# Performance work log

Measured on AMD Instinct MI355X. Metric: run time of the kernel, lower is better.

Reference implementation:

```python
import jax, jax.numpy as jnp
import numpy as np

B = 8192
FEAT = 7680
HID = 512
LOC = 4
N_SCENES = 72


def setup_inputs() -> dict:
    key = jax.random.key(0)
    ks = jax.random.split(key, 12)
    s = lambda fan_in: 1.0 / np.sqrt(fan_in)
    inp = {
        "feat": jax.random.normal(ks[0], (B, FEAT), dtype=jnp.float32),
        "scene_idx": jax.random.randint(ks[1], (B,), 0, N_SCENES, dtype=jnp.int64),
        # visual_fc1: Linear(7680 -> 512)  (torch layout: W[out, in])
        "W1": jax.random.uniform(ks[2], (HID, FEAT), jnp.float32, -s(FEAT), s(FEAT)),
        "b1": jax.random.uniform(ks[3], (HID,), jnp.float32, -s(FEAT), s(FEAT)),
        # localization_fc: Linear(512 -> 512), ReLU, Linear(512 -> 4)
        "W2": jax.random.uniform(ks[4], (HID, HID), jnp.float32, -s(HID), s(HID)),
        "b2": jax.random.uniform(ks[5], (HID,), jnp.float32, -s(HID), s(HID)),
        "W3": jax.random.uniform(ks[6], (LOC, HID), jnp.float32, -s(HID), s(HID)),
        "b3": jax.random.uniform(ks[7], (LOC,), jnp.float32, -s(HID), s(HID)),
        # per-scene 2x2 affine (with bias) and 2x2 rotation (no bias)
        "xyW": jax.random.uniform(ks[8], (N_SCENES, 2, 2), jnp.float32, -s(2), s(2)),
        "xyb": jax.random.uniform(ks[9], (N_SCENES, 2), jnp.float32, -s(2), s(2)),
        "tW": jax.random.uniform(ks[10], (N_SCENES, 2, 2), jnp.float32, -s(2), s(2)),
    }
    return inp


def reference(feat, scene_idx, W1, b1, W2, b2, W3, b3, xyW, xyb, tW):
    # visual_fc1: Flatten (already flat) -> Linear -> ReLU
    h = jax.nn.relu(feat @ W1.T + b1)                 # [B, HID]
    # localization_fc: Linear -> ReLU -> Linear
    h = jax.nn.relu(h @ W2.T + b2)                    # [B, HID]
    shared = h @ W3.T + b3                            # [B, 4]
    # per-scene routed 2x2 linears: gather weights per sample, apply, "scatter" is
    # implicit since every row gets exactly one scene's transform.
    sidx = scene_idx.astype(jnp.int32)
    Wxy = xyW[sidx]                                   # [B, 2, 2]
    bxy = xyb[sidx]                                   # [B, 2]
    Wt = tW[sidx]                                     # [B, 2, 2]
    xy = jnp.einsum("boi,bi->bo", Wxy, shared[:, :2]) + bxy
    t = jnp.einsum("boi,bi->bo", Wt, shared[:, 2:])
    return jnp.concatenate([xy, t], axis=1)           # [B, 4]
```

## Files before the change

### kernel.cpp

```cpp
#include <hip/hip_runtime.h>
#include <stdint.h>
#include <stddef.h>

#define BROWS 8192
#define FEATK 7680
#define HIDN  512

typedef __attribute__((ext_vector_type(8))) __bf16 bf16x8;
typedef __attribute__((ext_vector_type(4))) float f32x4;

__device__ __forceinline__ unsigned short f2b(float f) {
  unsigned int u = __float_as_uint(f);
  unsigned int r = (u + 0x7FFFu + ((u >> 16) & 1u)) >> 16;
  return (unsigned short)r;
}

__global__ void cvt_kernel(const float* __restrict__ src, unsigned short* __restrict__ dst, int n4) {
  int i = blockIdx.x * blockDim.x + threadIdx.x;
  int stride = gridDim.x * blockDim.x;
  for (; i < n4; i += stride) {
    float4 v = ((const float4*)src)[i];
    ushort4 o;
    o.x = f2b(v.x); o.y = f2b(v.y); o.z = f2b(v.z); o.w = f2b(v.w);
    ((ushort4*)dst)[i] = o;
  }
}

#define K1_BM 64
#define K1_BK 32

__global__ __launch_bounds__(256, 2) void gemm1_fused_splitk(
    const float* __restrict__ A,
    const unsigned short* __restrict__ Bm,
    float* __restrict__ P,
    int M, int N, int K, int klen) {
  __shared__ unsigned short As[2][K1_BM * K1_BK];
  __shared__ unsigned short Bs[2][HIDN * K1_BK];

  const int tid  = threadIdx.x;
  const int lane = tid & 63;
  const int wid  = tid >> 6;
  const int l16  = lane & 15;
  const int quad = lane >> 4;

  const int n       = blockIdx.x;
  const int xcd     = n & 7;
  const int slot    = n >> 3;
  const int kchunk  = xcd & 3;
  const int rowblk  = ((xcd >> 2) << 6) | slot;

  const int rowBase = rowblk * K1_BM;
  const int k_begin = kchunk * klen;
  const int nsteps  = klen / K1_BK;

  const int arow = tid >> 3;
  const int akq  = tid & 7;
  const int brow0 = (wid * 64 + lane) >> 2;
  const int bkk   = (lane & 3) << 3;

  f32x4 acc[4][8] = {};

  {
    const int k0 = k_begin;
#pragma unroll
    for (int it = 0; it < 2; ++it) {
      int row = it * 32 + arow;
      float4 v = *(const float4*)(A + (size_t)(rowBase + row) * K + k0 + akq * 4);
      ushort4 o;
      o.x = f2b(v.x); o.y = f2b(v.y); o.z = f2b(v.z); o.w = f2b(v.w);
      *(ushort4*)(&As[0][row * K1_BK + akq * 4]) = o;
    }
#pragma unroll
    for (int it = 0; it < 8; ++it) {
      int cb  = it * 256 + wid * 64;
      int row = it * 64 + brow0;
      const unsigned short* gb = Bm + (size_t)row * K + (k0 + bkk);
      __builtin_amdgcn_global_load_lds(
          (const __attribute__((address_space(1))) void*)gb,
          (__attribute__((address_space(3))) void*)(&Bs[0][cb * 8]), 16, 0, 0);
    }
  }
  __syncthreads();

  int cur = 0;
  for (int t = 0; t < nsteps; ++t) {
    const int nxt = cur ^ 1;
    const bool hasNext = (t + 1 < nsteps);
    float4 va0, va1;

    if (hasNext) {
      const int kn = k_begin + (t + 1) * K1_BK;
      va0 = *(const float4*)(A + (size_t)(rowBase + arow) * K + kn + akq * 4);
      va1 = *(const float4*)(A + (size_t)(rowBase + 32 + arow) * K + kn + akq * 4);
#pragma unroll
      for (int it = 0; it < 8; ++it) {
        int cb  = it * 256 + wid * 64;
        int row = it * 64 + brow0;
        const unsigned short* gb = Bm + (size_t)row * K + (kn + bkk);
        __builtin_amdgcn_global_load_lds(
            (const __attribute__((address_space(1))) void*)gb,
            (__attribute__((address_space(3))) void*)(&Bs[nxt][cb * 8]), 16, 0, 0);
      }
    }

    bf16x8 af[4], bfr[8];
#pragma unroll
    for (int mt = 0; mt < 4; ++mt)
      af[mt] = *(const bf16x8*)(&As[cur][(mt * 16 + l16) * K1_BK + quad * 8]);
#pragma unroll
    for (int nt = 0; nt < 8; ++nt)
      bfr[nt] = *(const bf16x8*)(&Bs[cur][(wid * 128 + nt * 16 + l16) * K1_BK + quad * 8]);
#pragma unroll
    for (int mt = 0; mt < 4; ++mt)
#pragma unroll
      for (int nt = 0; nt < 8; ++nt)
        acc[mt][nt] = __builtin_amdgcn_mfma_f32_16x16x32_bf16(af[mt], bfr[nt], acc[mt][nt], 0, 0, 0);

    if (hasNext) {
      ushort4 o0, o1;
      o0.x = f2b(va0.x); o0.y = f2b(va0.y); o0.z = f2b(va0.z); o0.w = f2b(va0.w);
      o1.x = f2b(va1.x); o1.y = f2b(va1.y); o1.z = f2b(va1.z); o1.w = f2b(va1.w);
      *(ushort4*)(&As[nxt][arow * K1_BK + akq * 4]) = o0;
      *(ushort4*)(&As[nxt][(32 + arow) * K1_BK + akq * 4]) = o1;
    }
    __syncthreads();
    cur = nxt;
  }

  float* outp = P + (size_t)kchunk * M * N;
#pragma unroll
  for (int mt = 0; mt < 4; ++mt) {
#pragma unroll
    for (int r = 0; r < 4; ++r) {
      int row = rowBase + mt * 16 + quad * 4 + r;
      float* cp = outp + (size_t)row * N + wid * 128 + l16;
#pragma unroll
      for (int nt = 0; nt < 8; ++nt) cp[nt * 16] = acc[mt][nt][r];
    }
  }
}

__global__ __launch_bounds__(256) void reduce4_bias_relu(
    const float* __restrict__ P, const float* __restrict__ bias,
    unsigned short* __restrict__ H, int MN4, int N4) {
  int i = blockIdx.x * blockDim.x + threadIdx.x;
  if (i >= MN4) return;
  const float4* p = (const float4*)P;
  float4 a = p[i];
  float4 b = p[i + MN4];
  float4 c = p[i + 2 * MN4];
  float4 d = p[i + 3 * MN4];
  float4 bs = ((const float4*)bias)[i % N4];
  ushort4 o;
  o.x = f2b(fmaxf(a.x + b.x + c.x + d.x + bs.x, 0.0f));
  o.y = f2b(fmaxf(a.y + b.y + c.y + d.y + bs.y, 0.0f));
  o.z = f2b(fmaxf(a.z + b.z + c.z + d.z + bs.z, 0.0f));
  o.w = f2b(fmaxf(a.w + b.w + c.w + d.w + bs.w, 0.0f));
  ((ushort4*)H)[i] = o;
}

#define K2_BM 64
#define K2_BN 128
#define K2_BK 64

__global__ __launch_bounds__(256, 2) void gemm2_bias_relu(
    const unsigned short* __restrict__ A,
    const unsigned short* __restrict__ Bm,
    const float* __restrict__ bias,
    unsigned short* __restrict__ C,
    int M, int N, int K) {
  __shared__ unsigned short As[2][K2_BM * K2_BK];
  __shared__ unsigned short Bs[2][K2_BN * K2_BK];
  const int tid  = threadIdx.x;
  const int lane = tid & 63;
  const int wid  = tid >> 6;
  const int wm   = wid >> 1;
  const int wn   = wid & 1;
  const int l16  = lane & 15;
  const int quad = lane >> 4;
  const int rowBase = blockIdx.y * K2_BM;
  const int colBase = blockIdx.x * K2_BN;

  const int srow = tid >> 3;
  const int skk  = (tid & 7) << 3;

  f32x4 acc[2][4] = {};
  const int nsteps = K / K2_BK;

#pragma unroll
  for (int it = 0; it < 2; ++it) {
    int cb  = it * 256 + wid * 64;
    int row = it * 32 + srow;
    const unsigned short* ga = A + (size_t)(rowBase + row) * K + skk;
    __builtin_amdgcn_global_load_lds(
        (const __attribute__((address_space(1))) void*)ga,
        (__attribute__((address_space(3))) void*)(&As[0][cb * 8]), 16, 0, 0);
  }
#pragma unroll
  for (int it = 0; it < 4; ++it) {
    int cb  = it * 256 + wid * 64;
    int row = it * 32 + srow;
    const unsigned short* gb = Bm + (size_t)(colBase + row) * K + skk;
    __builtin_amdgcn_global_load_lds(
        (const __attribute__((address_space(1))) void*)gb,
        (__attribute__((address_space(3))) void*)(&Bs[0][cb * 8]), 16, 0, 0);
  }
  __syncthreads();

  int cur = 0;
  for (int t = 0; t < nsteps; ++t) {
    const int nxt = cur ^ 1;
    if (t + 1 < nsteps) {
      const int kn = (t + 1) * K2_BK;
#pragma unroll
      for (int it = 0; it < 2; ++it) {
        int cb  = it * 256 + wid * 64;
        int row = it * 32 + srow;
        const unsigned short* ga = A + (size_t)(rowBase + row) * K + kn + skk;
        __builtin_amdgcn_global_load_lds(
            (const __attribute__((address_space(1))) void*)ga,
            (__attribute__((address_space(3))) void*)(&As[nxt][cb * 8]), 16, 0, 0);
      }
#pragma unroll
      for (int it = 0; it < 4; ++it) {
        int cb  = it * 256 + wid * 64;
        int row = it * 32 + srow;
        const unsigned short* gb = Bm + (size_t)(colBase + row) * K + kn + skk;
        __builtin_amdgcn_global_load_lds(
            (const __attribute__((address_space(1))) void*)gb,
            (__attribute__((address_space(3))) void*)(&Bs[nxt][cb * 8]), 16, 0, 0);
      }
    }
#pragma unroll
    for (int kk = 0; kk < K2_BK; kk += 32) {
      bf16x8 af[2], bfr[4];
#pragma unroll
      for (int mt = 0; mt < 2; ++mt)
        af[mt] = *(const bf16x8*)(&As[cur][(wm * 32 + mt * 16 + l16) * K2_BK + kk + quad * 8]);
#pragma unroll
      for (int nt = 0; nt < 4; ++nt)
        bfr[nt] = *(const bf16x8*)(&Bs[cur][(wn * 64 + nt * 16 + l16) * K2_BK + kk + quad * 8]);
#pragma unroll
      for (int mt = 0; mt < 2; ++mt)
#pragma unroll
        for (int nt = 0; nt < 4; ++nt)
          acc[mt][nt] = __builtin_amdgcn_mfma_f32_16x16x32_bf16(af[mt], bfr[nt], acc[mt][nt], 0, 0, 0);
    }
    __syncthreads();
    cur = nxt;
  }

  float bvals[4];
#pragma unroll
  for (int nt = 0; nt < 4; ++nt) bvals[nt] = bias[colBase + wn * 64 + nt * 16 + l16];
#pragma unroll
  for (int mt = 0; mt < 2; ++mt) {
#pragma unroll
    for (int r = 0; r < 4; ++r) {
      int row = rowBase + wm * 32 + mt * 16 + quad * 4 + r;
      unsigned short* cp = C + (size_t)row * N + colBase + wn * 64 + l16;
#pragma unroll
      for (int nt = 0; nt < 4; ++nt) {
        float v = fmaxf(acc[mt][nt][r] + bvals[nt], 0.0f);
        cp[nt * 16] = f2b(v);
      }
    }
  }
}

__global__ __launch_bounds__(256) void head_kernel(
    const unsigned short* __restrict__ h2,
    const float* __restrict__ W3,
    const float* __restrict__ b3,
    const int* __restrict__ sidx,
    const float* __restrict__ xyW,
    const float* __restrict__ xyb,
    const float* __restrict__ tW,
    float* __restrict__ out) {
  int wave = (blockIdx.x * blockDim.x + threadIdx.x) >> 6;
  int lane = threadIdx.x & 63;
  if (wave >= BROWS) return;

  bf16x8 hv = *(const bf16x8*)(h2 + (size_t)wave * 512 + lane * 8);
  float hf[8];
#pragma unroll
  for (int j = 0; j < 8; ++j) hf[j] = (float)hv[j];

  float s[4];
#pragma unroll
  for (int o = 0; o < 4; ++o) {
    const float* wrow = W3 + o * 512 + lane * 8;
    float4 w0 = ((const float4*)wrow)[0];
    float4 w1 = ((const float4*)wrow)[1];
    float a = hf[0] * w0.x + hf[1] * w0.y + hf[2] * w0.z + hf[3] * w0.w +
              hf[4] * w1.x + hf[5] * w1.y + hf[6] * w1.z + hf[7] * w1.w;
#pragma unroll
    for (int off = 32; off > 0; off >>= 1) a += __shfl_down(a, off, 64);
    s[o] = a;
  }

  if (lane == 0) {
#pragma unroll
    for (int o = 0; o < 4; ++o) s[o] += b3[o];
    int sc = sidx[wave];
    const float* wx = xyW + sc * 4;
    const float* bx = xyb + sc * 2;
    const float* wt = tW + sc * 4;
    float o0 = wx[0] * s[0] + wx[1] * s[1] + bx[0];
    float o1 = wx[2] * s[0] + wx[3] * s[1] + bx[1];
    float o2 = wt[0] * s[2] + wt[1] * s[3];
    float o3 = wt[2] * s[2] + wt[3] * s[3];
    ((float4*)out)[wave] = make_float4(o0, o1, o2, o3);
  }
}

#define WS_W1B   0UL
#define WS_W2B   7864320UL
#define WS_H1    8388608UL
#define WS_H2    16777216UL
#define WS_PART  25165824UL
#define WS_NEED  92274688UL

extern "C" void kernel_launch(void* const* d_in, const int* in_sizes, int n_in,
                              void* d_out, int out_size, void* d_ws, size_t ws_size,
                              hipStream_t stream) {
  const float* feat = (const float*)d_in[0];
  const int*   sidx = (const int*)d_in[1];
  const float* W1   = (const float*)d_in[2];
  const float* b1   = (const float*)d_in[3];
  const float* W2   = (const float*)d_in[4];
  const float* b2   = (const float*)d_in[5];
  const float* W3   = (const float*)d_in[6];
  const float* b3   = (const float*)d_in[7];
  const float* xyW  = (const float*)d_in[8];
  const float* xyb  = (const float*)d_in[9];
  const float* tW   = (const float*)d_in[10];
  float* out = (float*)d_out;

  if (ws_size < WS_NEED) return;

  char* ws = (char*)d_ws;
  unsigned short* W1B  = (unsigned short*)(ws + WS_W1B);
  unsigned short* W2B  = (unsigned short*)(ws + WS_W2B);
  unsigned short* h1   = (unsigned short*)(ws + WS_H1);
  unsigned short* h2   = (unsigned short*)(ws + WS_H2);
  float*          part = (float*)(ws + WS_PART);

  cvt_kernel<<<512, 256, 0, stream>>>(W1, W1B, (HIDN * FEATK) / 4);
  cvt_kernel<<<64, 256, 0, stream>>>(W2, W2B, (HIDN * HIDN) / 4);

  gemm1_fused_splitk<<<512, 256, 0, stream>>>(
      feat, W1B, part, BROWS, HIDN, FEATK, FEATK / 4);
  reduce4_bias_relu<<<(BROWS * HIDN / 4 + 255) / 256, 256, 0, stream>>>(
      part, b1, h1, BROWS * HIDN / 4, HIDN / 4);

  gemm2_bias_relu<<<dim3(HIDN / K2_BN, BROWS / K2_BM), 256, 0, stream>>>(
      h1, W2B, b2, h2, BROWS, HIDN, HIDN);

  head_kernel<<<(BROWS * 64) / 256, 256, 0, stream>>>(
      h2, W3, b3, sidx, xyW, xyb, tW, out);
}
```

Measured before the change: 479.9 us.

## Double GEMM1 row tile to 128 with 8-wave blocks and merge weight conversions

GEMM1 now uses 512-thread blocks that cover 128 rows, split 2x4 across waves, so each W1 tile staged in LDS is reused across twice as many rows and per-block B loading halves. The grid drops to 256 blocks, and the XCD-aware block-to-(row, k-chunk) mapping is replaced by a simple n&3 / n>>2 mapping. The two fp32-to-bf16 weight conversion launches are merged into one kernel to save a launch. LDS use doubles for the A tile and occupancy falls to one block per CU, and the loss of the XCD mapping may hurt L2 locality.

```diff
diff --git a/kernel.cpp b/kernel.cpp
--- a/kernel.cpp
+++ b/kernel.cpp
@@ -15,21 +15,25 @@
   return (unsigned short)r;
 }
 
-__global__ void cvt_kernel(const float* __restrict__ src, unsigned short* __restrict__ dst, int n4) {
+__global__ void cvt2_kernel(const float* __restrict__ s1, unsigned short* __restrict__ d1, int n1,
+                            const float* __restrict__ s2, unsigned short* __restrict__ d2, int n2) {
   int i = blockIdx.x * blockDim.x + threadIdx.x;
   int stride = gridDim.x * blockDim.x;
-  for (; i < n4; i += stride) {
-    float4 v = ((const float4*)src)[i];
+  for (; i < n1 + n2; i += stride) {
+    const float4* sp; ushort4* dp; int j;
+    if (i < n1) { sp = (const float4*)s1; dp = (ushort4*)d1; j = i; }
+    else        { sp = (const float4*)s2; dp = (ushort4*)d2; j = i - n1; }
+    float4 v = sp[j];
     ushort4 o;
     o.x = f2b(v.x); o.y = f2b(v.y); o.z = f2b(v.z); o.w = f2b(v.w);
-    ((ushort4*)dst)[i] = o;
-  }
-}
-
-#define K1_BM 64
+    dp[j] = o;
+  }
+}
+
+#define K1_BM 128
 #define K1_BK 32
 
-__global__ __launch_bounds__(256, 2) void gemm1_fused_splitk(
+__global__ __launch_bounds__(512, 1) void gemm1_fused_splitk(
     const float* __restrict__ A,
     const unsigned short* __restrict__ Bm,
     float* __restrict__ P,
@@ -40,21 +44,21 @@
   const int tid  = threadIdx.x;
   const int lane = tid & 63;
   const int wid  = tid >> 6;
+  const int wm   = wid >> 2;
+  const int wn   = wid & 3;
   const int l16  = lane & 15;
   const int quad = lane >> 4;
 
   const int n       = blockIdx.x;
-  const int xcd     = n & 7;
-  const int slot    = n >> 3;
-  const int kchunk  = xcd & 3;
-  const int rowblk  = ((xcd >> 2) << 6) | slot;
+  const int kchunk  = n & 3;
+  const int rowblk  = n >> 2;
 
   const int rowBase = rowblk * K1_BM;
   const int k_begin = kchunk * klen;
   const int nsteps  = klen / K1_BK;
 
-  const int arow = tid >> 3;
-  const int akq  = tid & 7;
+  const int arow  = tid >> 3;
+  const int akq   = tid & 7;
   const int brow0 = (wid * 64 + lane) >> 2;
   const int bkk   = (lane & 3) << 3;
 
@@ -64,16 +68,16 @@
     const int k0 = k_begin;
 #pragma unroll
     for (int it = 0; it < 2; ++it) {
-      int row = it * 32 + arow;
+      int row = it * 64 + arow;
       float4 v = *(const float4*)(A + (size_t)(rowBase + row) * K + k0 + akq * 4);
       ushort4 o;
       o.x = f2b(v.x); o.y = f2b(v.y); o.z = f2b(v.z); o.w = f2b(v.w);
       *(ushort4*)(&As[0][row * K1_BK + akq * 4]) = o;
     }
 #pragma unroll
-    for (int it = 0; it < 8; ++it) {
-      int cb  = it * 256 + wid * 64;
-      int row = it * 64 + brow0;
+    for (int it = 0; it < 4; ++it) {
+      int cb  = it * 512 + wid * 64;
+      int row = it * 128 + brow0;
       const unsigned short* gb = Bm + (size_t)row * K + (k0 + bkk);
       __builtin_amdgcn_global_load_lds(
           (const __attribute__((address_space(1))) void*)gb,
@@ -91,11 +95,11 @@
     if (hasNext) {
       const int kn = k_begin + (t + 1) * K1_BK;
       va0 = *(const float4*)(A + (size_t)(rowBase + arow) * K + kn + akq * 4);
-      va1 = *(const float4*)(A + (size_t)(rowBase + 32 + arow) * K + kn + akq * 4);
-#pragma unroll
-      for (int it = 0; it < 8; ++it) {
-        int cb  = it * 256 + wid * 64;
-        int row = it * 64 + brow0;
+      va1 = *(const float4*)(A + (size_t)(rowBase + 64 + arow) * K + kn + akq * 4);
+#pragma unroll
+      for (int it = 0; it < 4; ++it) {
+        int cb  = it * 512 + wid * 64;
+        int row = it * 128 + brow0;
         const unsigned short* gb = Bm + (size_t)row * K + (kn + bkk);
         __builtin_amdgcn_global_load_lds(
             (const __attribute__((address_space(1))) void*)gb,
@@ -106,10 +110,10 @@
     bf16x8 af[4], bfr[8];
 #pragma unroll
     for (int mt = 0; mt < 4; ++mt)
-      af[mt] = *(const bf16x8*)(&As[cur][(mt * 16 + l16) * K1_BK + quad * 8]);
+      af[mt] = *(const bf16x8*)(&As[cur][(wm * 64 + mt * 16 + l16) * K1_BK + quad * 8]);
 #pragma unroll
     for (int nt = 0; nt < 8; ++nt)
-      bfr[nt] = *(const bf16x8*)(&Bs[cur][(wid * 128 + nt * 16 + l16) * K1_BK + quad * 8]);
+      bfr[nt] = *(const bf16x8*)(&Bs[cur][(wn * 128 + nt * 16 + l16) * K1_BK + quad * 8]);
 #pragma unroll
     for (int mt = 0; mt < 4; ++mt)
 #pragma unroll
@@ -121,7 +125,7 @@
       o0.x = f2b(va0.x); o0.y = f2b(va0.y); o0.z = f2b(va0.z); o0.w = f2b(va0.w);
       o1.x = f2b(va1.x); o1.y = f2b(va1.y); o1.z = f2b(va1.z); o1.w = f2b(va1.w);
       *(ushort4*)(&As[nxt][arow * K1_BK + akq * 4]) = o0;
-      *(ushort4*)(&As[nxt][(32 + arow) * K1_BK + akq * 4]) = o1;
+      *(ushort4*)(&As[nxt][(64 + arow) * K1_BK + akq * 4]) = o1;
     }
     __syncthreads();
     cur = nxt;
@@ -132,8 +136,8 @@
   for (int mt = 0; mt < 4; ++mt) {
 #pragma unroll
     for (int r = 0; r < 4; ++r) {
-      int row = rowBase + mt * 16 + quad * 4 + r;
-      float* cp = outp + (size_t)row * N + wid * 128 + l16;
+      int row = rowBase + wm * 64 + mt * 16 + quad * 4 + r;
+      float* cp = outp + (size_t)row * N + wn * 128 + l16;
 #pragma unroll
       for (int nt = 0; nt < 8; ++nt) cp[nt * 16] = acc[mt][nt][r];
     }
@@ -346,10 +350,10 @@
   unsigned short* h2   = (unsigned short*)(ws + WS_H2);
   float*          part = (float*)(ws + WS_PART);
 
-  cvt_kernel<<<512, 256, 0, stream>>>(W1, W1B, (HIDN * FEATK) / 4);
-  cvt_kernel<<<64, 256, 0, stream>>>(W2, W2B, (HIDN * HIDN) / 4);
-
-  gemm1_fused_splitk<<<512, 256, 0, stream>>>(
+  cvt2_kernel<<<576, 256, 0, stream>>>(W1, W1B, (HIDN * FEATK) / 4,
+                                       W2, W2B, (HIDN * HIDN) / 4);
+
+  gemm1_fused_splitk<<<256, 512, 0, stream>>>(
       feat, W1B, part, BROWS, HIDN, FEATK, FEATK / 4);
   reduce4_bias_relu<<<(BROWS * HIDN / 4 + 255) / 256, 256, 0, stream>>>(
       part, b1, h1, BROWS * HIDN / 4, HIDN / 4);
```

Measured after the change: 467.7 us. -2.5%, faster.
